# Optimization experiments

Hardware: AMD Instinct MI355X
Metric: run time of the kernel (lower is better)

Reference implementation:

```python
import jax, jax.numpy as jnp
import numpy as np

B, N, D, H, DH, DFF = 2, 2048, 1024, 16, 64, 4096
EPS = 1e-5  # F.layer_norm default


def setup_inputs() -> dict:
    key = jax.random.key(0)
    ks = jax.random.split(key, 8)
    w = lambda k, shape: jax.random.normal(k, shape, dtype=jnp.float32) * 0.02
    # standard rotary frequencies over full head dim (rot_dim = DH)
    inv_freq = 1.0 / (10000.0 ** (jnp.arange(0, DH, 2, dtype=jnp.float32) / DH))
    t = jnp.arange(N, dtype=jnp.float32)
    f = t[:, None] * inv_freq[None, :]          # [N, DH/2]
    freqs = jnp.concatenate([f, f], axis=-1)    # [N, DH]
    return {
        "x": jax.random.normal(ks[0], (B, N, D), dtype=jnp.float32),
        "gamma_pre": jnp.ones((D,), jnp.float32),
        "w_qkv": w(ks[1], (3 * D, D)),
        "w_o": w(ks[2], (D, D)),
        "gamma_ff": jnp.ones((D,), jnp.float32),
        "w_up": w(ks[3], (DFF, D)),
        "b_up": jnp.zeros((DFF,), jnp.float32),
        "w_gate": w(ks[4], (DFF, D)),
        "b_gate": jnp.zeros((DFF,), jnp.float32),
        "w_out": w(ks[5], (D, DFF)),
        "b_out": jnp.zeros((D,), jnp.float32),
        "freqs": freqs,
        "mask": jnp.ones((B, N), dtype=bool),
    }


def _layernorm(x, gamma):
    mu = jnp.mean(x, axis=-1, keepdims=True)
    var = jnp.var(x, axis=-1, keepdims=True)
    return (x - mu) * jax.lax.rsqrt(var + EPS) * gamma


def _rotate_half(x):
    x1, x2 = jnp.split(x, 2, axis=-1)
    return jnp.concatenate([-x2, x1], axis=-1)


def _rope(t, freqs):
    # rot_dim == DH so nothing is left unrotated
    return t * jnp.cos(freqs) + _rotate_half(t) * jnp.sin(freqs)


def reference(x, gamma_pre, w_qkv, w_o, gamma_ff, w_up, b_up, w_gate, b_gate,
              w_out, b_out, freqs, mask):
    b, n, d = x.shape
    # ---- self-attention branch (pre-norm) ----
    h = _layernorm(x, gamma_pre)
    qkv = h @ w_qkv.T                                   # [b, n, 3d]
    q, k, v = jnp.split(qkv, 3, axis=-1)
    to_heads = lambda t: t.reshape(b, n, H, DH).transpose(0, 2, 1, 3)  # b h n d
    q, k, v = to_heads(q), to_heads(k), to_heads(v)
    q = _rope(q, freqs)
    k = _rope(k, freqs)
    scale = 1.0 / np.sqrt(DH).astype(np.float32)
    dots = jnp.einsum('bhid,bhjd->bhij', q, k) * scale  # [b, H, n, n]
    neg = -jnp.finfo(dots.dtype).max
    dots = jnp.where(mask[:, None, None, :], dots, neg)        # key padding mask
    causal = jnp.triu(jnp.ones((n, n), dtype=bool), 1)
    dots = jnp.where(causal, neg, dots)
    attn = jax.nn.softmax(dots.astype(jnp.float32), axis=-1).astype(dots.dtype)
    o = jnp.einsum('bhij,bhjd->bhid', attn, v)
    o = o.transpose(0, 2, 1, 3).reshape(b, n, d) @ w_o.T
    o = jnp.where(mask[..., None], o, 0.0)
    x = x + o
    # ---- GLU feed-forward branch (pre-norm) ----
    h2 = _layernorm(x, gamma_ff)
    up = h2 @ w_up.T + b_up
    gate = h2 @ w_gate.T + b_gate
    ff = (up * jax.nn.silu(gate)) @ w_out.T + b_out
    return x + ff
```

## Files before the change

### kernel.cpp

```cpp
#include <hip/hip_runtime.h>
#include <stdint.h>


#define B_ 2
#define N_ 2048
#define D_ 1024
#define H_ 16
#define DFF_ 4096
#define ROWS_ (B_*N_)

typedef unsigned short u16;
typedef short short4_ __attribute__((ext_vector_type(4)));
typedef short short8 __attribute__((ext_vector_type(8)));
typedef float float4_ __attribute__((ext_vector_type(4)));

#define NEGBIG (-1e30f)
#define QSCALE 0.1803368801111204f

__device__ __forceinline__ float b2f(u16 u) {
  union { unsigned u; float f; } c; c.u = ((unsigned)u) << 16; return c.f;
}
__device__ __forceinline__ u16 f2b(float f) {
  union { float f; unsigned u; } c; c.f = f;
  unsigned x = c.u;
  x += 0x7fffu + ((x >> 16) & 1u);
  return (u16)(x >> 16);
}

__device__ __forceinline__ void gl_lds16(const u16* g, u16* l) {
  __builtin_amdgcn_global_load_lds(
      (const __attribute__((address_space(1))) unsigned int*)g,
      (__attribute__((address_space(3))) unsigned int*)l, 16, 0, 0);
}

__global__ __launch_bounds__(256) void cvt_all(const float* __restrict__ s_qkv,
                                               const float* __restrict__ s_o,
                                               const float* __restrict__ s_up,
                                               const float* __restrict__ s_gate,
                                               const float* __restrict__ s_out,
                                               u16* __restrict__ d_qkv,
                                               u16* __restrict__ d_o,
                                               u16* __restrict__ d_up,
                                               u16* __restrict__ d_gate,
                                               u16* __restrict__ d_out_) {
  int c = blockIdx.x * 256 + threadIdx.x;
  const float* src; u16* dst; int off;
  if (c < 393216)       { src = s_qkv;  dst = d_qkv;  off = c; }
  else if (c < 524288)  { src = s_o;    dst = d_o;    off = c - 393216; }
  else if (c < 1048576) { src = s_up;   dst = d_up;   off = c - 524288; }
  else if (c < 1572864) { src = s_gate; dst = d_gate; off = c - 1048576; }
  else                  { src = s_out;  dst = d_out_; off = c - 1572864; }
  int i = off * 8;
  float4_ v0 = *(const float4_*)(src + i);
  float4_ v1 = *(const float4_*)(src + i + 4);
  short8 pk;
#pragma unroll
  for (int e = 0; e < 4; e++) { pk[e] = (short)f2b(v0[e]); pk[4 + e] = (short)f2b(v1[e]); }
  *(short8*)(dst + i) = pk;
}

__global__ __launch_bounds__(256) void ln_kernel(const float* __restrict__ xin,
                                                 const float* __restrict__ gamma,
                                                 u16* __restrict__ out) {
  int row = blockIdx.x, t = threadIdx.x;
  float4_ v = *(const float4_*)(xin + (size_t)row * D_ + t * 4);
  float s = 0.f, ss = 0.f;
#pragma unroll
  for (int i = 0; i < 4; i++) { s += v[i]; ss += v[i] * v[i]; }
#pragma unroll
  for (int off = 1; off < 64; off <<= 1) {
    s  += __shfl_xor(s, off, 64);
    ss += __shfl_xor(ss, off, 64);
  }
  __shared__ float red[8];
  if ((t & 63) == 0) { red[t >> 6] = s; red[4 + (t >> 6)] = ss; }
  __syncthreads();
  s  = red[0] + red[1] + red[2] + red[3];
  ss = red[4] + red[5] + red[6] + red[7];
  float mu  = s * (1.f / D_);
  float var = ss * (1.f / D_) - mu * mu;
  float rs  = rsqrtf(var + 1e-5f);
#pragma unroll
  for (int i = 0; i < 4; i++)
    out[(size_t)row * D_ + t * 4 + i] = f2b((v[i] - mu) * rs * gamma[t * 4 + i]);
}

__global__ __launch_bounds__(256) void combine_ln(const u16* p0,
                                                  const u16* __restrict__ p1,
                                                  const float* __restrict__ resid,
                                                  const float* __restrict__ gamma,
                                                  float* __restrict__ x1,
                                                  u16* h2out) {
  int row = blockIdx.x, t = threadIdx.x;
  size_t base = (size_t)row * D_ + t * 4;
  short4_ a = *(const short4_*)(p0 + base);
  short4_ b = *(const short4_*)(p1 + base);
  float4_ rv = *(const float4_*)(resid + base);
  float4_ v;
  float s = 0.f, ss = 0.f;
#pragma unroll
  for (int i = 0; i < 4; i++) {
    v[i] = b2f((u16)a[i]) + b2f((u16)b[i]) + rv[i];
    s += v[i]; ss += v[i] * v[i];
  }
  *(float4_*)(x1 + base) = v;
#pragma unroll
  for (int off = 1; off < 64; off <<= 1) {
    s  += __shfl_xor(s, off, 64);
    ss += __shfl_xor(ss, off, 64);
  }
  __shared__ float red[8];
  if ((t & 63) == 0) { red[t >> 6] = s; red[4 + (t >> 6)] = ss; }
  __syncthreads();
  s  = red[0] + red[1] + red[2] + red[3];
  ss = red[4] + red[5] + red[6] + red[7];
  float mu  = s * (1.f / D_);
  float var = ss * (1.f / D_) - mu * mu;
  float rs  = rsqrtf(var + 1e-5f);
#pragma unroll
  for (int i = 0; i < 4; i++)
    h2out[base + i] = f2b((v[i] - mu) * rs * gamma[t * 4 + i]);
}

template <int MODE>
__device__ __forceinline__ void gemm_epilogue(float4_ (&acc)[4][4], void* Cout,
                                              const float* bias, const void* extra,
                                              int mbase, int nbase, int N,
                                              int wr, int wc, int quad, int l16) {
#pragma unroll
  for (int i = 0; i < 4; i++) {
#pragma unroll
    for (int r = 0; r < 4; r++) {
      int row = mbase + wr * 64 + i * 16 + quad * 4 + r;
#pragma unroll
      for (int j = 0; j < 4; j++) {
        int col = nbase + wc * 64 + j * 16 + l16;
        size_t idx = (size_t)row * N + col;
        float v = acc[i][j][r];
        if (MODE == 0) {
          ((u16*)Cout)[idx] = f2b(v);
        } else if (MODE == 1) {
          ((u16*)Cout)[idx] = f2b(v + bias[col]);
        } else if (MODE == 2) {
          ((float*)Cout)[idx] = v + ((const float*)extra)[idx];
        } else if (MODE == 3) {
          float gate = v + bias[col];
          float sig = 1.f / (1.f + expf(-gate));
          float upv = b2f(((const u16*)extra)[idx]);
          ((u16*)Cout)[idx] = f2b(upv * gate * sig);
        } else {
          ((float*)Cout)[idx] = v + bias[col] + ((const float*)extra)[idx];
        }
      }
    }
  }
}

__device__ __forceinline__ void gemm_core64(const u16* A, const u16* W,
                                            float4_ (&acc)[4][4], u16* sA, u16* sW,
                                            int mbase, int nbase, int K,
                                            int klo, int khi,
                                            int wave, int lane, int wr, int wc,
                                            int quad, int l16) {
  int colb = ((lane & 3) ^ ((lane >> 3) & 3)) << 3;
  int qs8  = (quad ^ ((l16 >> 1) & 3)) * 8;
  for (int k0 = klo; k0 < khi; k0 += 64) {
    __syncthreads();
#pragma unroll
    for (int hh = 0; hh < 2; hh++) {
      int kh = k0 + hh * 32;
#pragma unroll
      for (int it = 0; it < 2; it++) {
        int c = wave * 128 + it * 64 + lane;
        int row = c >> 2;
        gl_lds16(A + (size_t)(mbase + row) * K + kh + colb,
                 sA + hh * 4096 + (size_t)(wave * 128 + it * 64) * 8);
        gl_lds16(W + (size_t)(nbase + row) * K + kh + colb,
                 sW + hh * 4096 + (size_t)(wave * 128 + it * 64) * 8);
      }
    }
    __syncthreads();
#pragma unroll
    for (int hh = 0; hh < 2; hh++) {
      const u16* sAp = sA + hh * 4096;
      const u16* sWp = sW + hh * 4096;
      short8 af[4], bf[4];
#pragma unroll
      for (int i = 0; i < 4; i++)
        af[i] = *(const short8*)(sAp + (wr * 64 + i * 16 + l16) * 32 + qs8);
#pragma unroll
      for (int j = 0; j < 4; j++)
        bf[j] = *(const short8*)(sWp + (wc * 64 + j * 16 + l16) * 32 + qs8);
#pragma unroll
      for (int i = 0; i < 4; i++)
#pragma unroll
        for (int j = 0; j < 4; j++)
          acc[i][j] = __builtin_amdgcn_mfma_f32_16x16x32_bf16(af[i], bf[j], acc[i][j], 0, 0, 0);
    }
  }
}

__global__ __launch_bounds__(256) void gemm_bb_split(const u16* __restrict__ A,
                                                     const u16* __restrict__ W,
                                                     u16* __restrict__ p0,
                                                     u16* __restrict__ p1,
                                                     int M, int N, int K) {
  __shared__ __align__(16) u16 sA[2][128 * 32];
  __shared__ __align__(16) u16 sW[2][128 * 32];
  int t = threadIdx.x;
  int mbase = blockIdx.y * 128, nbase = blockIdx.x * 128;
  int z = blockIdx.z;
  int wave = t >> 6, lane = t & 63;
  int wr = wave >> 1, wc = wave & 1;
  int quad = lane >> 4, l16 = lane & 15;
  int Kh = K >> 1;

  float4_ z4 = {0.f, 0.f, 0.f, 0.f};
  float4_ acc[4][4];
#pragma unroll
  for (int i = 0; i < 4; i++)
#pragma unroll
    for (int j = 0; j < 4; j++) acc[i][j] = z4;

  gemm_core64(A, W, acc, &sA[0][0], &sW[0][0], mbase, nbase, K,
              z * Kh, z * Kh + Kh, wave, lane, wr, wc, quad, l16);

  u16* P = z ? p1 : p0;
#pragma unroll
  for (int i = 0; i < 4; i++)
#pragma unroll
    for (int r = 0; r < 4; r++) {
      int row = mbase + wr * 64 + i * 16 + quad * 4 + r;
#pragma unroll
      for (int j = 0; j < 4; j++) {
        int col = nbase + wc * 64 + j * 16 + l16;
        P[(size_t)row * N + col] = f2b(acc[i][j][r]);
      }
    }
}

__device__ __forceinline__ void glu8_stageA(const u16* A, u16* aslot, int mbase,
                                            int kk, int wave, int lane, int colb) {
  int rw = wave * 16 + (lane >> 2);
#pragma unroll
  for (int it = 0; it < 2; it++) {
    int row = it * 128 + rw;
    gl_lds16(A + (size_t)(mbase + row) * 1024 + kk * 32 + colb,
             aslot + it * 4096 + wave * 512);
  }
}
__device__ __forceinline__ void glu8_stageB(const u16* Wu, const u16* Wg, u16* bslot,
                                            int nbase, int kk, int wave, int lane,
                                            int colb) {
  int rw = wave * 16 + (lane >> 2);
  size_t go = (size_t)(nbase + rw) * 1024 + kk * 32 + colb;
  gl_lds16(Wu + go, bslot + wave * 512);
  gl_lds16(Wg + go, bslot + 4096 + wave * 512);
}

__global__ __launch_bounds__(512) void gemm_glu8(const u16* __restrict__ A,
                                                 const u16* __restrict__ Wu,
                                                 const u16* __restrict__ Wg,
                                                 const float* __restrict__ bu,
                                                 const float* __restrict__ bg,
                                                 u16* __restrict__ G) {
  __shared__ __align__(16) u16 ring[4][16384];
  const int NT = 32;
  int t_ = threadIdx.x, wave = t_ >> 6, lane = t_ & 63;
  int wr = wave >> 2, wc = wave & 3;
  int quad = lane >> 4, l16 = lane & 15;
  int mbase = blockIdx.y * 256, nbase = blockIdx.x * 128;
  int colb = ((lane & 3) ^ ((lane >> 3) & 3)) << 3;
  int qs8  = (quad ^ ((l16 >> 1) & 3)) * 8;

  float4_ z4 = {0.f, 0.f, 0.f, 0.f};
  float4_ acc[8][4];
#pragma unroll
  for (int i = 0; i < 8; i++)
#pragma unroll
    for (int j = 0; j < 4; j++) acc[i][j] = z4;

#pragma unroll
  for (int kk = 0; kk < 3; kk++) {
    glu8_stageA(A, ring[kk], mbase, kk, wave, lane, colb);
    glu8_stageB(Wu, Wg, ring[kk] + 8192, nbase, kk, wave, lane, colb);
  }

  for (int t = 0; t < NT; t++) {
    if (t < NT - 2)       asm volatile("s_waitcnt vmcnt(8)" ::: "memory");
    else if (t == NT - 2) asm volatile("s_waitcnt vmcnt(4)" ::: "memory");
    else                  asm volatile("s_waitcnt vmcnt(0)" ::: "memory");
    __builtin_amdgcn_s_barrier();
    asm volatile("" ::: "memory");

    const u16* as = ring[t & 3];
    const u16* bs = as + 8192;
    bool prefetch = (t + 3 < NT);
    int kk = t + 3;

    if (prefetch) glu8_stageA(A, ring[kk & 3], mbase, kk, wave, lane, colb);
    short8 af[4], bf[4];
#pragma unroll
    for (int i = 0; i < 4; i++)
      af[i] = *(const short8*)(as + (wr * 128 + i * 16 + l16) * 32 + qs8);
#pragma unroll
    for (int j = 0; j < 4; j++)
      bf[j] = *(const short8*)(bs + (wc * 64 + j * 16 + l16) * 32 + qs8);
    __builtin_amdgcn_s_setprio(1);
#pragma unroll
    for (int i = 0; i < 4; i++)
#pragma unroll
      for (int j = 0; j < 4; j++)
        acc[i][j] = __builtin_amdgcn_mfma_f32_16x16x32_bf16(af[i], bf[j], acc[i][j], 0, 0, 0);
    __builtin_amdgcn_s_setprio(0);
    __builtin_amdgcn_s_barrier();
    asm volatile("" ::: "memory");

    if (prefetch) glu8_stageB(Wu, Wg, ring[kk & 3] + 8192, nbase, kk, wave, lane, colb);
    short8 ag[4];
#pragma unroll
    for (int i = 0; i < 4; i++)
      ag[i] = *(const short8*)(as + (wr * 128 + (4 + i) * 16 + l16) * 32 + qs8);
    __builtin_amdgcn_s_setprio(1);
#pragma unroll
    for (int i = 0; i < 4; i++)
#pragma unroll
      for (int j = 0; j < 4; j++)
        acc[4 + i][j] = __builtin_amdgcn_mfma_f32_16x16x32_bf16(ag[i], bf[j], acc[4 + i][j], 0, 0, 0);
    __builtin_amdgcn_s_setprio(0);
  }

  __syncthreads();
  u16* ex = &ring[0][0];
  if (wc >= 2) {
    int cc = (wc - 2) * 64;
#pragma unroll
    for (int i = 0; i < 8; i++)
#pragma unroll
      for (int r = 0; r < 4; r++) {
        int row = wr * 128 + i * 16 + quad * 4 + r;
#pragma unroll
        for (int j = 0; j < 4; j++) {
          int col = cc + j * 16 + l16;
          float gv = acc[i][j][r] + bg[nbase + col];
          float sig = 1.f / (1.f + expf(-gv));
          ex[row * 128 + col] = f2b(gv * sig);
        }
      }
  }
  __syncthreads();
  if (wc < 2) {
    int cc = wc * 64;
#pragma unroll
    for (int i = 0; i < 8; i++)
#pragma unroll
      for (int r = 0; r < 4; r++) {
        int row = wr * 128 + i * 16 + quad * 4 + r;
#pragma unroll
        for (int j = 0; j < 4; j++) {
          int col = cc + j * 16 + l16;
          float uv = acc[i][j][r] + bu[nbase + col];
          G[(size_t)(mbase + row) * DFF_ + nbase + col] =
              f2b(uv * b2f(ex[row * 128 + col]));
        }
      }
  }
}

__global__ __launch_bounds__(256) void split_combine(const u16* __restrict__ p0,
                                                     const u16* __restrict__ p1,
                                                     const float* __restrict__ bias,
                                                     const float* __restrict__ resid,
                                                     float* __restrict__ out, int N) {
  int idx = (blockIdx.x * 256 + threadIdx.x) * 8;
  int col = idx & (N - 1);
  short8 a = *(const short8*)(p0 + idx);
  short8 b = *(const short8*)(p1 + idx);
  float4_ r0 = *(const float4_*)(resid + idx);
  float4_ r1 = *(const float4_*)(resid + idx + 4);
  float4_ o0, o1;
#pragma unroll
  for (int e = 0; e < 4; e++) {
    float bb0 = bias ? bias[col + e] : 0.f;
    float bb1 = bias ? bias[col + 4 + e] : 0.f;
    o0[e] = b2f((u16)a[e]) + b2f((u16)b[e]) + bb0 + r0[e];
    o1[e] = b2f((u16)a[4 + e]) + b2f((u16)b[4 + e]) + bb1 + r1[e];
  }
  *(float4_*)(out + idx) = o0;
  *(float4_*)(out + idx + 4) = o1;
}

template <int MODE>
__global__ __launch_bounds__(256) void gemm_nt(const u16* __restrict__ A,
                                               const float* __restrict__ W,
                                               void* Cout,
                                               const float* __restrict__ bias,
                                               const void* extra,
                                               int M, int N, int K) {
  __shared__ __align__(16) u16 sA[128 * 32];
  __shared__ __align__(16) u16 sW[128 * 32];
  int t = threadIdx.x;
  int mbase = blockIdx.y * 128, nbase = blockIdx.x * 128;
  int wave = t >> 6, lane = t & 63;
  int wr = wave >> 1, wc = wave & 1;
  int quad = lane >> 4, l16 = lane & 15;

  float4_ z4 = {0.f, 0.f, 0.f, 0.f};
  float4_ acc[4][4];
#pragma unroll
  for (int i = 0; i < 4; i++)
#pragma unroll
    for (int j = 0; j < 4; j++) acc[i][j] = z4;

  for (int k0 = 0; k0 < K; k0 += 32) {
    __syncthreads();
#pragma unroll
    for (int it = 0; it < 2; it++) {
      int c = t + 256 * it;
      int row = c >> 2, col = (c & 3) << 3;
      ((short8*)sA)[c] = *(const short8*)(A + (size_t)(mbase + row) * K + k0 + col);
      const float* wp = W + (size_t)(nbase + row) * K + k0 + col;
      float4_ w0 = *(const float4_*)wp;
      float4_ w1 = *(const float4_*)(wp + 4);
      short8 pk;
#pragma unroll
      for (int e = 0; e < 4; e++) { pk[e] = (short)f2b(w0[e]); pk[4 + e] = (short)f2b(w1[e]); }
      ((short8*)sW)[c] = pk;
    }
    __syncthreads();
    short8 af[4], bf[4];
#pragma unroll
    for (int i = 0; i < 4; i++)
      af[i] = *(const short8*)(sA + (wr * 64 + i * 16 + l16) * 32 + quad * 8);
#pragma unroll
    for (int j = 0; j < 4; j++)
      bf[j] = *(const short8*)(sW + (wc * 64 + j * 16 + l16) * 32 + quad * 8);
#pragma unroll
    for (int i = 0; i < 4; i++)
#pragma unroll
      for (int j = 0; j < 4; j++)
        acc[i][j] = __builtin_amdgcn_mfma_f32_16x16x32_bf16(af[i], bf[j], acc[i][j], 0, 0, 0);
  }
  gemm_epilogue<MODE>(acc, Cout, bias, extra, mbase, nbase, N, wr, wc, quad, l16);
}

template <int SPLIT>
__global__ __launch_bounds__(256) void rope_kernel(const u16* __restrict__ q0,
                                                   const u16* __restrict__ q1,
                                                   const float* __restrict__ freqs,
                                                   u16* __restrict__ qr,
                                                   u16* __restrict__ kr,
                                                   u16* __restrict__ vt) {
  int idx = blockIdx.x * 256 + threadIdx.x;
  int d2 = idx & 31;
  int h  = (idx >> 5) & 15;
  int n  = (idx >> 9) & 2047;
  int b  = idx >> 20;
  float f = freqs[n * 64 + d2];
  float c = cosf(f), s = sinf(f);
  size_t base = (size_t)(b * N_ + n) * 3072;
  int hd = h * 64 + d2;
#define LD(o) (SPLIT ? (b2f(q0[base + (o)]) + b2f(q1[base + (o)])) : b2f(q0[base + (o)]))
  float v_q1 = LD(hd),        v_q2 = LD(hd + 32);
  float v_k1 = LD(1024 + hd), v_k2 = LD(1024 + hd + 32);
  float v_v1 = LD(2048 + hd), v_v2 = LD(2048 + hd + 32);
#undef LD
  size_t ro = ((size_t)(b * H_ + h) * N_ + n) * 64 + d2;
  qr[ro]      = f2b((v_q1 * c - v_q2 * s) * QSCALE);
  qr[ro + 32] = f2b((v_q2 * c + v_q1 * s) * QSCALE);
  kr[ro]      = f2b(v_k1 * c - v_k2 * s);
  kr[ro + 32] = f2b(v_k2 * c + v_k1 * s);
  size_t vo = ((size_t)(b * H_ + h) * 64 + d2) * N_ + n;
  vt[vo]           = f2b(v_v1);
  vt[vo + 32 * N_] = f2b(v_v2);
}

#define LP 72
#define NSPLIT 4
__global__ __launch_bounds__(256) void attn_kernel(const u16* __restrict__ qr,
                                                   const u16* __restrict__ kr,
                                                   const u16* __restrict__ vt,
                                                   u16* __restrict__ opart,
                                                   float* __restrict__ mlp) {
  __shared__ __align__(16) u16 sK[64 * LP];
  __shared__ __align__(16) u16 sV[64 * LP];
  __shared__ __align__(16) u16 sP[4][16 * LP];
  int qp = blockIdx.x, bh = blockIdx.y, sp = blockIdx.z;
  int t = threadIdx.x, wave = t >> 6, lane = t & 63;
  int quad = lane >> 4, l16 = lane & 15;
  const u16* qptr = qr + (size_t)bh * N_ * 64;
  const u16* kp = kr + (size_t)bh * N_ * 64;
  const u16* vp = vt + (size_t)bh * 64 * N_;
  float4_ z4 = {0.f, 0.f, 0.f, 0.f};
  short8 onesv;
#pragma unroll
  for (int e = 0; e < 8; e++) onesv[e] = (short)0x3F80;

  for (int qsel = 0; qsel < 2; qsel++) {
    int qt = qsel ? (N_ / 64 - 1 - qp) : qp;
    int qbase = qt * 64;
    int ntiles = qt + 1;
    int ktlo = (ntiles * sp) / NSPLIT, kthi = (ntiles * (sp + 1)) / NSPLIT;

    short8 aq[2];
    int qrow = qbase + wave * 16 + l16;
#pragma unroll
    for (int kk = 0; kk < 2; kk++)
      aq[kk] = *(const short8*)(qptr + (size_t)qrow * 64 + kk * 32 + quad * 8);

    float4_ o[4] = {z4, z4, z4, z4};
    float m_r[4] = {NEGBIG, NEGBIG, NEGBIG, NEGBIG};
    float l_r[4] = {0.f, 0.f, 0.f, 0.f};

    for (int kt = ktlo; kt < kthi; kt++) {
      __syncthreads();
      {
        const u16* src = kp + (size_t)kt * 64 * 64;
#pragma unroll
        for (int it = 0; it < 2; it++) {
          int c = t + 256 * it;
          int row = c >> 3, seg = c & 7;
          *(short8*)(sK + row * LP + seg * 8) = *(const short8*)(src + c * 8);
          *(short8*)(sV + row * LP + seg * 8) =
              *(const short8*)(vp + (size_t)row * N_ + kt * 64 + seg * 8);
        }
      }
      __syncthreads();

      float4_ sf[4];
#pragma unroll
      for (int j = 0; j < 4; j++) {
        short8 bk0 = *(const short8*)(sK + (j * 16 + l16) * LP + quad * 8);
        short8 bk1 = *(const short8*)(sK + (j * 16 + l16) * LP + 32 + quad * 8);
        float4_ acc = z4;
        acc = __builtin_amdgcn_mfma_f32_16x16x32_bf16(aq[0], bk0, acc, 0, 0, 0);
        acc = __builtin_amdgcn_mfma_f32_16x16x32_bf16(aq[1], bk1, acc, 0, 0, 0);
        sf[j] = acc;
      }
      if (kt == qt) {
#pragma unroll
        for (int j = 0; j < 4; j++)
#pragma unroll
          for (int r = 0; r < 4; r++) {
            int ig = qbase + wave * 16 + quad * 4 + r;
            int jg = kt * 64 + j * 16 + l16;
            if (jg > ig) sf[j][r] = NEGBIG;
          }
      }

      float alpha_r[4];
#pragma unroll
      for (int r = 0; r < 4; r++) {
        float mt = fmaxf(fmaxf(sf[0][r], sf[1][r]), fmaxf(sf[2][r], sf[3][r]));
#pragma unroll
        for (int off = 1; off < 16; off <<= 1) mt = fmaxf(mt, __shfl_xor(mt, off, 64));
        float mn = fmaxf(m_r[r], mt);
        alpha_r[r] = exp2f(m_r[r] - mn);
        m_r[r] = mn;
#pragma unroll
        for (int j = 0; j < 4; j++) sf[j][r] = exp2f(sf[j][r] - mn);
#pragma unroll
        for (int jo = 0; jo < 4; jo++) o[jo][r] *= alpha_r[r];
      }

      u16* sPw = sP[wave];
#pragma unroll
      for (int j = 0; j < 4; j++)
#pragma unroll
        for (int r = 0; r < 4; r++)
          sPw[(quad * 4 + r) * LP + j * 16 + l16] = f2b(sf[j][r]);
      short8 ap[2];
#pragma unroll
      for (int kk = 0; kk < 2; kk++)
        ap[kk] = *(const short8*)(sPw + l16 * LP + kk * 32 + quad * 8);

      float4_ ls = z4;
      ls = __builtin_amdgcn_mfma_f32_16x16x32_bf16(ap[0], onesv, ls, 0, 0, 0);
      ls = __builtin_amdgcn_mfma_f32_16x16x32_bf16(ap[1], onesv, ls, 0, 0, 0);
#pragma unroll
      for (int r = 0; r < 4; r++) l_r[r] = l_r[r] * alpha_r[r] + ls[r];

#pragma unroll
      for (int jo = 0; jo < 4; jo++)
#pragma unroll
        for (int kk = 0; kk < 2; kk++) {
          short8 bv = *(const short8*)(sV + (jo * 16 + l16) * LP + kk * 32 + quad * 8);
          o[jo] = __builtin_amdgcn_mfma_f32_16x16x32_bf16(ap[kk], bv, o[jo], 0, 0, 0);
        }
    }

#pragma unroll
    for (int r = 0; r < 4; r++) {
      int n = qbase + wave * 16 + quad * 4 + r;
      size_t row = (size_t)bh * N_ + n;
      if (l16 == 0) {
        mlp[2 * (sp * (size_t)65536 + row)]     = m_r[r];
        mlp[2 * (sp * (size_t)65536 + row) + 1] = l_r[r];
      }
#pragma unroll
      for (int jo = 0; jo < 4; jo++)
        opart[sp * (size_t)4194304 + row * 64 + jo * 16 + l16] = f2b(o[jo][r]);
    }
  }
}

__global__ __launch_bounds__(256) void attn_combine(const u16* __restrict__ opart,
                                                    const float* __restrict__ mlp,
                                                    u16* __restrict__ obuf) {
  int idx = blockIdx.x * 256 + threadIdx.x;
  int row = idx >> 3, seg = idx & 7;
  float mm[NSPLIT], ll[NSPLIT];
  float mmax = NEGBIG;
#pragma unroll
  for (int s = 0; s < NSPLIT; s++) {
    mm[s] = mlp[2 * (s * (size_t)65536 + row)];
    ll[s] = mlp[2 * (s * (size_t)65536 + row) + 1];
    mmax = fmaxf(mmax, mm[s]);
  }
  float w[NSPLIT], lsum = 0.f;
#pragma unroll
  for (int s = 0; s < NSPLIT; s++) { w[s] = exp2f(mm[s] - mmax); lsum += ll[s] * w[s]; }
  float inv = 1.f / lsum;
  float acc[8] = {0, 0, 0, 0, 0, 0, 0, 0};
#pragma unroll
  for (int s = 0; s < NSPLIT; s++) {
    short8 a = *(const short8*)(opart + s * (size_t)4194304 + (size_t)row * 64 + seg * 8);
#pragma unroll
    for (int e = 0; e < 8; e++) acc[e] += b2f((u16)a[e]) * w[s];
  }
  short8 r;
#pragma unroll
  for (int e = 0; e < 8; e++) r[e] = (short)f2b(acc[e] * inv);
  int bh = row >> 11, n = row & 2047;
  int bb = bh >> 4, h = bh & 15;
  *(short8*)(obuf + ((size_t)(bb * N_ + n) * D_) + h * 64 + seg * 8) = r;
}

extern "C" void kernel_launch(void* const* d_in, const int* in_sizes, int n_in,
                              void* d_out, int out_size, void* d_ws, size_t ws_size,
                              hipStream_t stream) {
  const float* x         = (const float*)d_in[0];
  const float* gamma_pre = (const float*)d_in[1];
  const float* w_qkv     = (const float*)d_in[2];
  const float* w_o       = (const float*)d_in[3];
  const float* gamma_ff  = (const float*)d_in[4];
  const float* w_up      = (const float*)d_in[5];
  const float* b_up      = (const float*)d_in[6];
  const float* w_gate    = (const float*)d_in[7];
  const float* b_gate    = (const float*)d_in[8];
  const float* w_out     = (const float*)d_in[9];
  const float* b_out     = (const float*)d_in[10];
  const float* freqs     = (const float*)d_in[11];

  char* ws = (char*)d_ws;
  const size_t MB = 1024 * 1024;
  float* out = (float*)d_out;
  bool wide = ws_size >= 96 * MB;

  if (wide) {
    u16*  h     = (u16*)(ws);
    u16*  qp0   = (u16*)(ws + 8 * MB);
    u16*  qp1   = (u16*)(ws + 32 * MB);
    u16*  qr    = (u16*)(ws + 56 * MB);
    u16*  kr    = (u16*)d_out;
    u16*  vtb   = (u16*)d_out + 4194304;
    u16*  opart = (u16*)(ws);
    float* mlb  = (float*)(ws + 32 * MB);
    u16*  ob    = (u16*)(ws + 34 * MB);
    u16*  sp0   = (u16*)(ws);
    u16*  sp1o  = (u16*)(ws + 8 * MB);
    float* x1   = (float*)(ws + 16 * MB);
    u16*  h2    = (u16*)(ws);
    u16*  g     = (u16*)(ws + 32 * MB);
    u16*  sp0f  = (u16*)(ws);
    u16*  sp1f  = (u16*)(ws + 8 * MB);
    u16* wb_qkv  = (u16*)(ws + 64 * MB);
    u16* wb_o    = (u16*)(ws + 70 * MB);
    u16* wb_up   = (u16*)(ws + 72 * MB);
    u16* wb_gate = (u16*)(ws + 80 * MB);
    u16* wb_out  = (u16*)(ws + 88 * MB);

    cvt_all<<<8192, 256, 0, stream>>>(w_qkv, w_o, w_up, w_gate, w_out,
                                      wb_qkv, wb_o, wb_up, wb_gate, wb_out);
    ln_kernel<<<ROWS_, 256, 0, stream>>>(x, gamma_pre, h);
    gemm_bb_split<<<dim3(3072 / 128, ROWS_ / 128, 2), 256, 0, stream>>>(
        h, wb_qkv, qp0, qp1, ROWS_, 3072, 1024);
    rope_kernel<1><<<(B_ * N_ * H_ * 32) / 256, 256, 0, stream>>>(
        qp0, qp1, freqs, qr, kr, vtb);
    attn_kernel<<<dim3(N_ / 128, B_ * H_, NSPLIT), 256, 0, stream>>>(
        qr, kr, vtb, opart, mlb);
    attn_combine<<<(B_ * H_ * N_ * 8) / 256, 256, 0, stream>>>(opart, mlb, ob);
    gemm_bb_split<<<dim3(1024 / 128, ROWS_ / 128, 2), 256, 0, stream>>>(
        ob, wb_o, sp0, sp1o, ROWS_, 1024, 1024);
    combine_ln<<<ROWS_, 256, 0, stream>>>(sp0, sp1o, x, gamma_ff, x1, h2);
    gemm_glu8<<<dim3(DFF_ / 128, ROWS_ / 256), 512, 0, stream>>>(
        h2, wb_up, wb_gate, b_up, b_gate, g);
    gemm_bb_split<<<dim3(1024 / 128, ROWS_ / 128, 2), 256, 0, stream>>>(
        g, wb_out, sp0f, sp1f, ROWS_, 1024, 4096);
    split_combine<<<(ROWS_ * 1024) / 2048, 256, 0, stream>>>(
        sp0f, sp1f, b_out, x1, out, 1024);
  } else {
    u16*  h     = (u16*)(ws);
    u16*  qkv   = (u16*)(ws + 8 * MB);
    u16*  qr    = (u16*)(ws + 32 * MB);
    u16*  kr    = (u16*)(ws + 40 * MB);
    u16*  vtb   = (u16*)(ws + 48 * MB);
    u16*  ob    = (u16*)(ws + 56 * MB);
    float* x1   = (float*)(ws + 8 * MB);
    u16*  h2    = (u16*)(ws + 24 * MB);
    u16*  g     = (u16*)(ws + 32 * MB);

    ln_kernel<<<ROWS_, 256, 0, stream>>>(x, gamma_pre, h);
    gemm_nt<0><<<dim3(3072 / 128, ROWS_ / 128), 256, 0, stream>>>(
        h, w_qkv, qkv, nullptr, nullptr, ROWS_, 3072, 1024);
    rope_kernel<0><<<(B_ * N_ * H_ * 32) / 256, 256, 0, stream>>>(
        qkv, qkv, freqs, qr, kr, vtb);
    attn_kernel<<<dim3(N_ / 128, B_ * H_, NSPLIT), 256, 0, stream>>>(
        qr, kr, vtb, (u16*)(ws), (float*)(ws + 32 * MB));
    attn_combine<<<(B_ * H_ * N_ * 8) / 256, 256, 0, stream>>>(
        (u16*)(ws), (float*)(ws + 32 * MB), ob);
    gemm_nt<2><<<dim3(1024 / 128, ROWS_ / 128), 256, 0, stream>>>(
        ob, w_o, x1, nullptr, x, ROWS_, 1024, 1024);
    ln_kernel<<<ROWS_, 256, 0, stream>>>(x1, gamma_ff, h2);
    gemm_nt<1><<<dim3(4096 / 128, ROWS_ / 128), 256, 0, stream>>>(
        h2, w_up, g, b_up, nullptr, ROWS_, 4096, 1024);
    gemm_nt<3><<<dim3(4096 / 128, ROWS_ / 128), 256, 0, stream>>>(
        h2, w_gate, g, b_gate, g, ROWS_, 4096, 1024);
    gemm_nt<4><<<dim3(1024 / 128, ROWS_ / 128), 256, 0, stream>>>(
        g, w_out, (void*)out, b_out, x1, ROWS_, 1024, 4096);
  }
}
```

Before: 452.5 us.

## Skip softmax rescale when max grows little; use unsplit QKV GEMM

The attention inner loop now rescales the running max and output accumulators only when a tile's row max exceeds the running max by more than 8 (in log2 units), checked wave-wide. Otherwise it reuses the stale max and skips the shuffles and the alpha multiplies. Separately, the QKV projection switches from the K-split GEMM plus a combining rope pass to a single non-split GEMM, which removes a partial-sum write and read. The lazy rescale lets unnormalised exponentials grow up to 2^8, which bf16 P can hold. The non-split GEMM has half as many blocks, which lowers parallelism.

```diff
diff --git a/kernel.cpp b/kernel.cpp
--- a/kernel.cpp
+++ b/kernel.cpp
@@ -198,6 +198,41 @@
           acc[i][j] = __builtin_amdgcn_mfma_f32_16x16x32_bf16(af[i], bf[j], acc[i][j], 0, 0, 0);
     }
   }
+}
+
+__global__ __launch_bounds__(256) void gemm_bb(const u16* __restrict__ A,
+                                               const u16* __restrict__ W,
+                                               u16* __restrict__ C,
+                                               int M, int N, int K) {
+  __shared__ __align__(16) u16 sA[2][128 * 32];
+  __shared__ __align__(16) u16 sW[2][128 * 32];
+  int t = threadIdx.x;
+  int mbase = blockIdx.y * 128, nbase = blockIdx.x * 128;
+  int wave = t >> 6, lane = t & 63;
+  int wr = wave >> 1, wc = wave & 1;
+  int quad = lane >> 4, l16 = lane & 15;
+
+  float4_ z4 = {0.f, 0.f, 0.f, 0.f};
+  float4_ acc[4][4];
+#pragma unroll
+  for (int i = 0; i < 4; i++)
+#pragma unroll
+    for (int j = 0; j < 4; j++) acc[i][j] = z4;
+
+  gemm_core64(A, W, acc, &sA[0][0], &sW[0][0], mbase, nbase, K,
+              0, K, wave, lane, wr, wc, quad, l16);
+
+#pragma unroll
+  for (int i = 0; i < 4; i++)
+#pragma unroll
+    for (int r = 0; r < 4; r++) {
+      int row = mbase + wr * 64 + i * 16 + quad * 4 + r;
+#pragma unroll
+      for (int j = 0; j < 4; j++) {
+        int col = nbase + wc * 64 + j * 16 + l16;
+        C[(size_t)row * N + col] = f2b(acc[i][j][r]);
+      }
+    }
 }
 
 __global__ __launch_bounds__(256) void gemm_bb_split(const u16* __restrict__ A,
@@ -548,20 +583,32 @@
           }
       }
 
-      float alpha_r[4];
-#pragma unroll
-      for (int r = 0; r < 4; r++) {
-        float mt = fmaxf(fmaxf(sf[0][r], sf[1][r]), fmaxf(sf[2][r], sf[3][r]));
-#pragma unroll
-        for (int off = 1; off < 16; off <<= 1) mt = fmaxf(mt, __shfl_xor(mt, off, 64));
-        float mn = fmaxf(m_r[r], mt);
-        alpha_r[r] = exp2f(m_r[r] - mn);
-        m_r[r] = mn;
-#pragma unroll
-        for (int j = 0; j < 4; j++) sf[j][r] = exp2f(sf[j][r] - mn);
-#pragma unroll
-        for (int jo = 0; jo < 4; jo++) o[jo][r] *= alpha_r[r];
-      }
+      float alpha_r[4], mt_r[4];
+#pragma unroll
+      for (int r = 0; r < 4; r++)
+        mt_r[r] = fmaxf(fmaxf(sf[0][r], sf[1][r]), fmaxf(sf[2][r], sf[3][r]));
+      bool need = (mt_r[0] > m_r[0] + 8.f) || (mt_r[1] > m_r[1] + 8.f) ||
+                  (mt_r[2] > m_r[2] + 8.f) || (mt_r[3] > m_r[3] + 8.f);
+      if (__any(need)) {
+#pragma unroll
+        for (int r = 0; r < 4; r++) {
+          float mt = mt_r[r];
+#pragma unroll
+          for (int off = 1; off < 16; off <<= 1) mt = fmaxf(mt, __shfl_xor(mt, off, 64));
+          float mn = fmaxf(m_r[r], mt);
+          alpha_r[r] = exp2f(m_r[r] - mn);
+          m_r[r] = mn;
+#pragma unroll
+          for (int jo = 0; jo < 4; jo++) o[jo][r] *= alpha_r[r];
+        }
+      } else {
+#pragma unroll
+        for (int r = 0; r < 4; r++) alpha_r[r] = 1.f;
+      }
+#pragma unroll
+      for (int r = 0; r < 4; r++)
+#pragma unroll
+        for (int j = 0; j < 4; j++) sf[j][r] = exp2f(sf[j][r] - m_r[r]);
 
       u16* sPw = sP[wave];
 #pragma unroll
@@ -659,8 +706,7 @@
 
   if (wide) {
     u16*  h     = (u16*)(ws);
-    u16*  qp0   = (u16*)(ws + 8 * MB);
-    u16*  qp1   = (u16*)(ws + 32 * MB);
+    u16*  qkv   = (u16*)(ws + 8 * MB);
     u16*  qr    = (u16*)(ws + 56 * MB);
     u16*  kr    = (u16*)d_out;
     u16*  vtb   = (u16*)d_out + 4194304;
@@ -683,10 +729,10 @@
     cvt_all<<<8192, 256, 0, stream>>>(w_qkv, w_o, w_up, w_gate, w_out,
                                       wb_qkv, wb_o, wb_up, wb_gate, wb_out);
     ln_kernel<<<ROWS_, 256, 0, stream>>>(x, gamma_pre, h);
-    gemm_bb_split<<<dim3(3072 / 128, ROWS_ / 128, 2), 256, 0, stream>>>(
-        h, wb_qkv, qp0, qp1, ROWS_, 3072, 1024);
-    rope_kernel<1><<<(B_ * N_ * H_ * 32) / 256, 256, 0, stream>>>(
-        qp0, qp1, freqs, qr, kr, vtb);
+    gemm_bb<<<dim3(3072 / 128, ROWS_ / 128), 256, 0, stream>>>(
+        h, wb_qkv, qkv, ROWS_, 3072, 1024);
+    rope_kernel<0><<<(B_ * N_ * H_ * 32) / 256, 256, 0, stream>>>(
+        qkv, qkv, freqs, qr, kr, vtb);
     attn_kernel<<<dim3(N_ / 128, B_ * H_, NSPLIT), 256, 0, stream>>>(
         qr, kr, vtb, opart, mlb);
     attn_combine<<<(B_ * H_ * N_ * 8) / 256, 256, 0, stream>>>(opart, mlb, ob);
```

New measurement: 450.2 us. About the same (-0.5%).
